# Kernel optimization log

Measured on AMD Instinct MI355X. Metric: run time of the kernel, lower is better.

Reference implementation:

```python
import jax, jax.numpy as jnp
import numpy as np

D_TENSOR = 64
SCALE = float(np.sqrt(D_TENSOR))


def setup_inputs() -> dict:
    key = jax.random.key(0)
    kq, kk, kv = jax.random.split(key, 3)
    shape = (1, 16, 4096, 64)  # [B, H, S, D]
    return {
        "q": jax.random.normal(kq, shape, dtype=jnp.float32),
        "k": jax.random.normal(kk, shape, dtype=jnp.float32),
        "v": jax.random.normal(kv, shape, dtype=jnp.float32),
    }


def reference(q, k, v):
    # attn = softmax(q @ k^T / sqrt(d)); output = attn @ v  (no mask, dropout=0/eval)
    scores = jnp.einsum("bhqd,bhkd->bhqk", q, k) / SCALE  # [B,H,S,S]
    attn = jax.nn.softmax(scores, axis=-1)
    output = jnp.einsum("bhqk,bhkd->bhqd", attn, v)       # [B,H,S,D]
    return (output, attn)
```

## Files before the change

### kernel.cpp

```cpp
#include <hip/hip_runtime.h>
#include <hip/hip_bf16.h>


#define NH  16
#define SEQ 4096
#define DH  64
#define BM  128
#define BN  64
#define NKT (SEQ / BN)
#define NRB (SEQ / BM)
#define NT  512

typedef __attribute__((ext_vector_type(8))) short bf16x8;
typedef __attribute__((ext_vector_type(4))) float f32x4;

static __device__ __forceinline__ unsigned short f2bf(float f) {
  unsigned x = __float_as_uint(f);
  return (unsigned short)((x + 0x7fffu + ((x >> 16) & 1u)) >> 16);
}

static __device__ __forceinline__ void bar_lgkm() {
  asm volatile("s_waitcnt lgkmcnt(0)" ::: "memory");
  __builtin_amdgcn_s_barrier();
  asm volatile("" ::: "memory");
}

static __device__ __forceinline__ int swz(int row, int col) {
  return row * 64 + (col ^ ((row & 7) << 3));
}


__global__ __launch_bounds__(NT, 4)
void attn_fused(const float* __restrict__ q, const float* __restrict__ kg,
                const float* __restrict__ vg, float* __restrict__ out,
                float* __restrict__ attn)
{
  __shared__ __align__(16) unsigned short Ks[2][64 * 64];
  __shared__ __align__(16) unsigned short Vt[2][64 * 64];
  __shared__ __align__(16) unsigned short Pb[4][32 * 64];

  const int nwg = NH * NRB;
  int bid = blockIdx.x;
  int wg = (bid & 7) * (nwg >> 3) + (bid >> 3);
  const int h    = wg >> 5;
  const int row0 = (wg & (NRB - 1)) * BM;

  const int t    = threadIdx.x;
  const int lane = t & 63;
  const int wid  = t >> 6;
  const int r16  = lane & 15;
  const int g4   = lane >> 4;
  const bool producer = (wid >= 4);

  const float* qh = q  + (size_t)h * SEQ * DH;
  const float* kh = kg + (size_t)h * SEQ * DH;
  const float* vh = vg + (size_t)h * SEQ * DH;

  const int pt = t - 256;
  const int pk = (pt & 255) >> 4;
  const int pd = (t & 15) * 4;

  bf16x8 qa[2][2];
  if (!producer) {
    const float QS = 0.125f * 1.44269504088896340736f;
    #pragma unroll
    for (int qf = 0; qf < 2; ++qf) {
      #pragma unroll
      for (int kf = 0; kf < 2; ++kf) {
        const float* qp = qh + (size_t)(row0 + wid * 32 + qf * 16 + r16) * DH + kf * 32 + g4 * 8;
        float4 x0 = *(const float4*)qp;
        float4 x1 = *(const float4*)(qp + 4);
        bf16x8 a;
        a[0] = (short)f2bf(x0.x * QS); a[1] = (short)f2bf(x0.y * QS);
        a[2] = (short)f2bf(x0.z * QS); a[3] = (short)f2bf(x0.w * QS);
        a[4] = (short)f2bf(x1.x * QS); a[5] = (short)f2bf(x1.y * QS);
        a[6] = (short)f2bf(x1.z * QS); a[7] = (short)f2bf(x1.w * QS);
        qa[qf][kf] = a;
      }
    }
  }

  float4 kr[4], vr[4];

  float rsum0 = 0.f, rsum1 = 0.f;

  if (producer) {
    #pragma unroll
    for (int i = 0; i < 4; ++i)
      kr[i] = *(const float4*)(kh + (size_t)(i * 16 + pk) * DH + pd);
    #pragma unroll
    for (int i = 0; i < 4; ++i)
      *(short4*)&Ks[0][swz(i * 16 + pk, pd)] =
          make_short4((short)f2bf(kr[i].x), (short)f2bf(kr[i].y),
                      (short)f2bf(kr[i].z), (short)f2bf(kr[i].w));
    #pragma unroll
    for (int i = 0; i < 4; ++i)
      kr[i] = *(const float4*)(kh + (size_t)(BN + i * 16 + pk) * DH + pd);
  }
  bar_lgkm();

  #pragma unroll 1
  for (int kt = 0; kt < NKT; ++kt) {
    if (producer) {
      if (kt < NKT - 1) {
        #pragma unroll
        for (int i = 0; i < 4; ++i)
          *(short4*)&Ks[(kt + 1) & 1][swz(i * 16 + pk, pd)] =
              make_short4((short)f2bf(kr[i].x), (short)f2bf(kr[i].y),
                          (short)f2bf(kr[i].z), (short)f2bf(kr[i].w));
        if (kt < NKT - 2) {
          #pragma unroll
          for (int i = 0; i < 4; ++i)
            kr[i] = *(const float4*)(kh + (size_t)((kt + 2) * BN + i * 16 + pk) * DH + pd);
        }
      }
    } else {
      const int b = kt & 1;
      #pragma unroll
      for (int n = 0; n < 4; ++n) {
        bf16x8 a0 = *(const bf16x8*)&Ks[b][swz(n * 16 + r16, g4 * 8)];
        bf16x8 a1 = *(const bf16x8*)&Ks[b][swz(n * 16 + r16, 32 + g4 * 8)];
        f32x4 c0 = {0.f, 0.f, 0.f, 0.f};
        f32x4 c1 = {0.f, 0.f, 0.f, 0.f};
        c0 = __builtin_amdgcn_mfma_f32_16x16x32_bf16(a0, qa[0][0], c0, 0, 0, 0);
        c0 = __builtin_amdgcn_mfma_f32_16x16x32_bf16(a1, qa[0][1], c0, 0, 0, 0);
        c1 = __builtin_amdgcn_mfma_f32_16x16x32_bf16(a0, qa[1][0], c1, 0, 0, 0);
        c1 = __builtin_amdgcn_mfma_f32_16x16x32_bf16(a1, qa[1][1], c1, 0, 0, 0);
        #pragma unroll
        for (int r = 0; r < 4; ++r) {
          rsum0 += __builtin_amdgcn_exp2f(c0[r]);
          rsum1 += __builtin_amdgcn_exp2f(c1[r]);
        }
      }
    }
    bar_lgkm();
  }

  float inv0 = 0.f, inv1 = 0.f;
  if (!producer) {
    rsum0 += __shfl_xor(rsum0, 16); rsum0 += __shfl_xor(rsum0, 32);
    rsum1 += __shfl_xor(rsum1, 16); rsum1 += __shfl_xor(rsum1, 32);
    inv0 = 1.0f / rsum0;
    inv1 = 1.0f / rsum1;
  }

  f32x4 accO[2][4];
  #pragma unroll
  for (int qf = 0; qf < 2; ++qf)
    #pragma unroll
    for (int n = 0; n < 4; ++n) accO[qf][n] = (f32x4){0.f, 0.f, 0.f, 0.f};

  if (producer) {
    #pragma unroll
    for (int i = 0; i < 4; ++i) {
      kr[i] = *(const float4*)(kh + (size_t)(i * 16 + pk) * DH + pd);
      vr[i] = *(const float4*)(vh + (size_t)(i * 16 + pk) * DH + pd);
    }
    #pragma unroll
    for (int i = 0; i < 4; ++i) {
      *(short4*)&Ks[0][swz(i * 16 + pk, pd)] =
          make_short4((short)f2bf(kr[i].x), (short)f2bf(kr[i].y),
                      (short)f2bf(kr[i].z), (short)f2bf(kr[i].w));
      Vt[0][swz(pd + 0, i * 16 + pk)] = f2bf(vr[i].x);
      Vt[0][swz(pd + 1, i * 16 + pk)] = f2bf(vr[i].y);
      Vt[0][swz(pd + 2, i * 16 + pk)] = f2bf(vr[i].z);
      Vt[0][swz(pd + 3, i * 16 + pk)] = f2bf(vr[i].w);
    }
    #pragma unroll
    for (int i = 0; i < 4; ++i) {
      kr[i] = *(const float4*)(kh + (size_t)(BN + i * 16 + pk) * DH + pd);
      vr[i] = *(const float4*)(vh + (size_t)(BN + i * 16 + pk) * DH + pd);
    }
  }
  bar_lgkm();

  float* ap0 = attn + (size_t)(h * SEQ + row0 + wid * 32 + r16) * SEQ;
  float* ap1 = ap0 + (size_t)16 * SEQ;

  #pragma unroll 1
  for (int kt = 0; kt < NKT; ++kt) {
    if (producer) {
      if (kt < NKT - 1) {
        const int b1 = (kt + 1) & 1;
        #pragma unroll
        for (int i = 0; i < 4; ++i) {
          *(short4*)&Ks[b1][swz(i * 16 + pk, pd)] =
              make_short4((short)f2bf(kr[i].x), (short)f2bf(kr[i].y),
                          (short)f2bf(kr[i].z), (short)f2bf(kr[i].w));
          Vt[b1][swz(pd + 0, i * 16 + pk)] = f2bf(vr[i].x);
          Vt[b1][swz(pd + 1, i * 16 + pk)] = f2bf(vr[i].y);
          Vt[b1][swz(pd + 2, i * 16 + pk)] = f2bf(vr[i].z);
          Vt[b1][swz(pd + 3, i * 16 + pk)] = f2bf(vr[i].w);
        }
        if (kt < NKT - 2) {
          #pragma unroll
          for (int i = 0; i < 4; ++i) {
            kr[i] = *(const float4*)(kh + (size_t)((kt + 2) * BN + i * 16 + pk) * DH + pd);
            vr[i] = *(const float4*)(vh + (size_t)((kt + 2) * BN + i * 16 + pk) * DH + pd);
          }
        }
      }
    } else {
      const int b = kt & 1;
      #pragma unroll
      for (int n = 0; n < 4; ++n) {
        bf16x8 a0 = *(const bf16x8*)&Ks[b][swz(n * 16 + r16, g4 * 8)];
        bf16x8 a1 = *(const bf16x8*)&Ks[b][swz(n * 16 + r16, 32 + g4 * 8)];
        f32x4 c0 = {0.f, 0.f, 0.f, 0.f};
        f32x4 c1 = {0.f, 0.f, 0.f, 0.f};
        c0 = __builtin_amdgcn_mfma_f32_16x16x32_bf16(a0, qa[0][0], c0, 0, 0, 0);
        c0 = __builtin_amdgcn_mfma_f32_16x16x32_bf16(a1, qa[0][1], c0, 0, 0, 0);
        c1 = __builtin_amdgcn_mfma_f32_16x16x32_bf16(a0, qa[1][0], c1, 0, 0, 0);
        c1 = __builtin_amdgcn_mfma_f32_16x16x32_bf16(a1, qa[1][1], c1, 0, 0, 0);
        f32x4 p0, p1;
        p0[0] = __builtin_amdgcn_exp2f(c0[0]) * inv0;
        p0[1] = __builtin_amdgcn_exp2f(c0[1]) * inv0;
        p0[2] = __builtin_amdgcn_exp2f(c0[2]) * inv0;
        p0[3] = __builtin_amdgcn_exp2f(c0[3]) * inv0;
        p1[0] = __builtin_amdgcn_exp2f(c1[0]) * inv1;
        p1[1] = __builtin_amdgcn_exp2f(c1[1]) * inv1;
        p1[2] = __builtin_amdgcn_exp2f(c1[2]) * inv1;
        p1[3] = __builtin_amdgcn_exp2f(c1[3]) * inv1;
        __builtin_nontemporal_store(p0, (f32x4*)(ap0 + (size_t)kt * BN + n * 16 + g4 * 4));
        __builtin_nontemporal_store(p1, (f32x4*)(ap1 + (size_t)kt * BN + n * 16 + g4 * 4));
        *(short4*)&Pb[wid][swz(r16, n * 16 + g4 * 4)] =
            make_short4((short)f2bf(p0[0]), (short)f2bf(p0[1]),
                        (short)f2bf(p0[2]), (short)f2bf(p0[3]));
        *(short4*)&Pb[wid][swz(16 + r16, n * 16 + g4 * 4)] =
            make_short4((short)f2bf(p1[0]), (short)f2bf(p1[1]),
                        (short)f2bf(p1[2]), (short)f2bf(p1[3]));
      }
      bf16x8 pa00 = *(const bf16x8*)&Pb[wid][swz(r16, g4 * 8)];
      bf16x8 pa01 = *(const bf16x8*)&Pb[wid][swz(r16, 32 + g4 * 8)];
      bf16x8 pa10 = *(const bf16x8*)&Pb[wid][swz(16 + r16, g4 * 8)];
      bf16x8 pa11 = *(const bf16x8*)&Pb[wid][swz(16 + r16, 32 + g4 * 8)];
      #pragma unroll
      for (int n = 0; n < 4; ++n) {
        bf16x8 v0 = *(const bf16x8*)&Vt[b][swz(n * 16 + r16, g4 * 8)];
        bf16x8 v1 = *(const bf16x8*)&Vt[b][swz(n * 16 + r16, 32 + g4 * 8)];
        accO[0][n] = __builtin_amdgcn_mfma_f32_16x16x32_bf16(pa00, v0, accO[0][n], 0, 0, 0);
        accO[0][n] = __builtin_amdgcn_mfma_f32_16x16x32_bf16(pa01, v1, accO[0][n], 0, 0, 0);
        accO[1][n] = __builtin_amdgcn_mfma_f32_16x16x32_bf16(pa10, v0, accO[1][n], 0, 0, 0);
        accO[1][n] = __builtin_amdgcn_mfma_f32_16x16x32_bf16(pa11, v1, accO[1][n], 0, 0, 0);
      }
    }
    bar_lgkm();
  }

  if (!producer) {
    #pragma unroll
    for (int qf = 0; qf < 2; ++qf) {
      #pragma unroll
      for (int n = 0; n < 4; ++n) {
        #pragma unroll
        for (int r = 0; r < 4; ++r) {
          __builtin_nontemporal_store(accO[qf][n][r],
              out + (size_t)(h * SEQ + row0 + wid * 32 + qf * 16 + g4 * 4 + r) * DH + n * 16 + r16);
        }
      }
    }
  }
}

extern "C" void kernel_launch(void* const* d_in, const int* in_sizes, int n_in,
                              void* d_out, int out_size, void* d_ws, size_t ws_size,
                              hipStream_t stream) {
  const float* q = (const float*)d_in[0];
  const float* k = (const float*)d_in[1];
  const float* v = (const float*)d_in[2];
  float* out  = (float*)d_out;
  float* attn = out + (size_t)NH * SEQ * DH;
  hipLaunchKernelGGL(attn_fused, dim3(NH * NRB), dim3(NT), 0, stream,
                     q, k, v, out, attn);
}
```

Before: 377.0 us.

## Drop producer/consumer warp split; all warps compute 256-row blocks and cooperatively load K/V

```diff
diff --git a/kernel.cpp b/kernel.cpp
--- a/kernel.cpp
+++ b/kernel.cpp
@@ -5,7 +5,7 @@
 #define NH  16
 #define SEQ 4096
 #define DH  64
-#define BM  128
+#define BM  256
 #define BN  64
 #define NKT (SEQ / BN)
 #define NRB (SEQ / BM)
@@ -37,12 +37,12 @@
 {
   __shared__ __align__(16) unsigned short Ks[2][64 * 64];
   __shared__ __align__(16) unsigned short Vt[2][64 * 64];
-  __shared__ __align__(16) unsigned short Pb[4][32 * 64];
+  __shared__ __align__(16) unsigned short Pb[8][32 * 64];
 
   const int nwg = NH * NRB;
   int bid = blockIdx.x;
   int wg = (bid & 7) * (nwg >> 3) + (bid >> 3);
-  const int h    = wg >> 5;
+  const int h    = wg >> 4;
   const int row0 = (wg & (NRB - 1)) * BM;
 
   const int t    = threadIdx.x;
@@ -50,72 +50,60 @@
   const int wid  = t >> 6;
   const int r16  = lane & 15;
   const int g4   = lane >> 4;
-  const bool producer = (wid >= 4);
+  const bool khalf = (wid < 4);
 
   const float* qh = q  + (size_t)h * SEQ * DH;
   const float* kh = kg + (size_t)h * SEQ * DH;
   const float* vh = vg + (size_t)h * SEQ * DH;
 
-  const int pt = t - 256;
-  const int pk = (pt & 255) >> 4;
-  const int pd = (t & 15) * 4;
-
+  const int kKey1 = t >> 4;
+  const int kD1   = (t & 15) * 4;
+
+  const int ku  = t & 255;
+  const int kk2 = ku >> 4;
+  const int kd2 = (ku & 15) * 4;
+  const int vk0 = (ku >> 4) * 4;
+  const int vd  = ku & 15;
+
+  const float QS = 0.125f * 1.44269504088896340736f;
   bf16x8 qa[2][2];
-  if (!producer) {
-    const float QS = 0.125f * 1.44269504088896340736f;
-    #pragma unroll
-    for (int qf = 0; qf < 2; ++qf) {
-      #pragma unroll
-      for (int kf = 0; kf < 2; ++kf) {
-        const float* qp = qh + (size_t)(row0 + wid * 32 + qf * 16 + r16) * DH + kf * 32 + g4 * 8;
-        float4 x0 = *(const float4*)qp;
-        float4 x1 = *(const float4*)(qp + 4);
-        bf16x8 a;
-        a[0] = (short)f2bf(x0.x * QS); a[1] = (short)f2bf(x0.y * QS);
-        a[2] = (short)f2bf(x0.z * QS); a[3] = (short)f2bf(x0.w * QS);
-        a[4] = (short)f2bf(x1.x * QS); a[5] = (short)f2bf(x1.y * QS);
-        a[6] = (short)f2bf(x1.z * QS); a[7] = (short)f2bf(x1.w * QS);
-        qa[qf][kf] = a;
-      }
-    }
-  }
-
-  float4 kr[4], vr[4];
+  #pragma unroll
+  for (int qf = 0; qf < 2; ++qf) {
+    #pragma unroll
+    for (int kf = 0; kf < 2; ++kf) {
+      const float* qp = qh + (size_t)(row0 + wid * 32 + qf * 16 + r16) * DH + kf * 32 + g4 * 8;
+      float4 x0 = *(const float4*)qp;
+      float4 x1 = *(const float4*)(qp + 4);
+      bf16x8 a;
+      a[0] = (short)f2bf(x0.x * QS); a[1] = (short)f2bf(x0.y * QS);
+      a[2] = (short)f2bf(x0.z * QS); a[3] = (short)f2bf(x0.w * QS);
+      a[4] = (short)f2bf(x1.x * QS); a[5] = (short)f2bf(x1.y * QS);
+      a[6] = (short)f2bf(x1.z * QS); a[7] = (short)f2bf(x1.w * QS);
+      qa[qf][kf] = a;
+    }
+  }
 
   float rsum0 = 0.f, rsum1 = 0.f;
-
-  if (producer) {
-    #pragma unroll
-    for (int i = 0; i < 4; ++i)
-      kr[i] = *(const float4*)(kh + (size_t)(i * 16 + pk) * DH + pd);
-    #pragma unroll
-    for (int i = 0; i < 4; ++i)
-      *(short4*)&Ks[0][swz(i * 16 + pk, pd)] =
-          make_short4((short)f2bf(kr[i].x), (short)f2bf(kr[i].y),
-                      (short)f2bf(kr[i].z), (short)f2bf(kr[i].w));
-    #pragma unroll
-    for (int i = 0; i < 4; ++i)
-      kr[i] = *(const float4*)(kh + (size_t)(BN + i * 16 + pk) * DH + pd);
-  }
-  bar_lgkm();
-
-  #pragma unroll 1
-  for (int kt = 0; kt < NKT; ++kt) {
-    if (producer) {
-      if (kt < NKT - 1) {
-        #pragma unroll
-        for (int i = 0; i < 4; ++i)
-          *(short4*)&Ks[(kt + 1) & 1][swz(i * 16 + pk, pd)] =
-              make_short4((short)f2bf(kr[i].x), (short)f2bf(kr[i].y),
-                          (short)f2bf(kr[i].z), (short)f2bf(kr[i].w));
-        if (kt < NKT - 2) {
-          #pragma unroll
-          for (int i = 0; i < 4; ++i)
-            kr[i] = *(const float4*)(kh + (size_t)((kt + 2) * BN + i * 16 + pk) * DH + pd);
-        }
-      }
-    } else {
+  {
+    float4 kr[2];
+    #pragma unroll
+    for (int i = 0; i < 2; ++i)
+      kr[i] = *(const float4*)(kh + (size_t)(kKey1 + 32 * i) * DH + kD1);
+
+    #pragma unroll 1
+    for (int kt = 0; kt < NKT; ++kt) {
       const int b = kt & 1;
+      #pragma unroll
+      for (int i = 0; i < 2; ++i)
+        *(short4*)&Ks[b][swz(kKey1 + 32 * i, kD1)] =
+            make_short4((short)f2bf(kr[i].x), (short)f2bf(kr[i].y),
+                        (short)f2bf(kr[i].z), (short)f2bf(kr[i].w));
+      if (kt + 1 < NKT) {
+        #pragma unroll
+        for (int i = 0; i < 2; ++i)
+          kr[i] = *(const float4*)(kh + (size_t)((kt + 1) * BN + kKey1 + 32 * i) * DH + kD1);
+      }
+      bar_lgkm();
       #pragma unroll
       for (int n = 0; n < 4; ++n) {
         bf16x8 a0 = *(const bf16x8*)&Ks[b][swz(n * 16 + r16, g4 * 8)];
@@ -132,17 +120,14 @@
           rsum1 += __builtin_amdgcn_exp2f(c1[r]);
         }
       }
-    }
-    bar_lgkm();
-  }
-
-  float inv0 = 0.f, inv1 = 0.f;
-  if (!producer) {
-    rsum0 += __shfl_xor(rsum0, 16); rsum0 += __shfl_xor(rsum0, 32);
-    rsum1 += __shfl_xor(rsum1, 16); rsum1 += __shfl_xor(rsum1, 32);
-    inv0 = 1.0f / rsum0;
-    inv1 = 1.0f / rsum1;
-  }
+      bar_lgkm();
+    }
+  }
+
+  rsum0 += __shfl_xor(rsum0, 16); rsum0 += __shfl_xor(rsum0, 32);
+  rsum1 += __shfl_xor(rsum1, 16); rsum1 += __shfl_xor(rsum1, 32);
+  const float inv0 = 1.0f / rsum0;
+  const float inv1 = 1.0f / rsum1;
 
   f32x4 accO[2][4];
   #pragma unroll
@@ -150,113 +135,108 @@
     #pragma unroll
     for (int n = 0; n < 4; ++n) accO[qf][n] = (f32x4){0.f, 0.f, 0.f, 0.f};
 
-  if (producer) {
-    #pragma unroll
-    for (int i = 0; i < 4; ++i) {
-      kr[i] = *(const float4*)(kh + (size_t)(i * 16 + pk) * DH + pd);
-      vr[i] = *(const float4*)(vh + (size_t)(i * 16 + pk) * DH + pd);
-    }
-    #pragma unroll
-    for (int i = 0; i < 4; ++i) {
-      *(short4*)&Ks[0][swz(i * 16 + pk, pd)] =
-          make_short4((short)f2bf(kr[i].x), (short)f2bf(kr[i].y),
-                      (short)f2bf(kr[i].z), (short)f2bf(kr[i].w));
-      Vt[0][swz(pd + 0, i * 16 + pk)] = f2bf(vr[i].x);
-      Vt[0][swz(pd + 1, i * 16 + pk)] = f2bf(vr[i].y);
-      Vt[0][swz(pd + 2, i * 16 + pk)] = f2bf(vr[i].z);
-      Vt[0][swz(pd + 3, i * 16 + pk)] = f2bf(vr[i].w);
-    }
-    #pragma unroll
-    for (int i = 0; i < 4; ++i) {
-      kr[i] = *(const float4*)(kh + (size_t)(BN + i * 16 + pk) * DH + pd);
-      vr[i] = *(const float4*)(vh + (size_t)(BN + i * 16 + pk) * DH + pd);
-    }
-  }
-  bar_lgkm();
+  float4 pre[4];
+  if (khalf) {
+    #pragma unroll
+    for (int i = 0; i < 4; ++i)
+      pre[i] = *(const float4*)(kh + (size_t)(kk2 + 16 * i) * DH + kd2);
+  } else {
+    #pragma unroll
+    for (int c = 0; c < 4; ++c) {
+      const float* vp = vh + (size_t)vk0 * DH + (vd + 16 * c);
+      pre[c].x = vp[0 * DH]; pre[c].y = vp[1 * DH];
+      pre[c].z = vp[2 * DH]; pre[c].w = vp[3 * DH];
+    }
+  }
+  __syncthreads();
 
   float* ap0 = attn + (size_t)(h * SEQ + row0 + wid * 32 + r16) * SEQ;
   float* ap1 = ap0 + (size_t)16 * SEQ;
 
   #pragma unroll 1
   for (int kt = 0; kt < NKT; ++kt) {
-    if (producer) {
-      if (kt < NKT - 1) {
-        const int b1 = (kt + 1) & 1;
-        #pragma unroll
-        for (int i = 0; i < 4; ++i) {
-          *(short4*)&Ks[b1][swz(i * 16 + pk, pd)] =
-              make_short4((short)f2bf(kr[i].x), (short)f2bf(kr[i].y),
-                          (short)f2bf(kr[i].z), (short)f2bf(kr[i].w));
-          Vt[b1][swz(pd + 0, i * 16 + pk)] = f2bf(vr[i].x);
-          Vt[b1][swz(pd + 1, i * 16 + pk)] = f2bf(vr[i].y);
-          Vt[b1][swz(pd + 2, i * 16 + pk)] = f2bf(vr[i].z);
-          Vt[b1][swz(pd + 3, i * 16 + pk)] = f2bf(vr[i].w);
+    const int b = kt & 1;
+    if (khalf) {
+      #pragma unroll
+      for (int i = 0; i < 4; ++i)
+        *(short4*)&Ks[b][swz(kk2 + 16 * i, kd2)] =
+            make_short4((short)f2bf(pre[i].x), (short)f2bf(pre[i].y),
+                        (short)f2bf(pre[i].z), (short)f2bf(pre[i].w));
+    } else {
+      #pragma unroll
+      for (int c = 0; c < 4; ++c)
+        *(short4*)&Vt[b][swz(vd + 16 * c, vk0)] =
+            make_short4((short)f2bf(pre[c].x), (short)f2bf(pre[c].y),
+                        (short)f2bf(pre[c].z), (short)f2bf(pre[c].w));
+    }
+    if (kt + 1 < NKT) {
+      if (khalf) {
+        #pragma unroll
+        for (int i = 0; i < 4; ++i)
+          pre[i] = *(const float4*)(kh + (size_t)((kt + 1) * BN + kk2 + 16 * i) * DH + kd2);
+      } else {
+        #pragma unroll
+        for (int c = 0; c < 4; ++c) {
+          const float* vp = vh + (size_t)((kt + 1) * BN + vk0) * DH + (vd + 16 * c);
+          pre[c].x = vp[0 * DH]; pre[c].y = vp[1 * DH];
+          pre[c].z = vp[2 * DH]; pre[c].w = vp[3 * DH];
         }
-        if (kt < NKT - 2) {
-          #pragma unroll
-          for (int i = 0; i < 4; ++i) {
-            kr[i] = *(const float4*)(kh + (size_t)((kt + 2) * BN + i * 16 + pk) * DH + pd);
-            vr[i] = *(const float4*)(vh + (size_t)((kt + 2) * BN + i * 16 + pk) * DH + pd);
-          }
-        }
-      }
-    } else {
-      const int b = kt & 1;
-      #pragma unroll
-      for (int n = 0; n < 4; ++n) {
-        bf16x8 a0 = *(const bf16x8*)&Ks[b][swz(n * 16 + r16, g4 * 8)];
-        bf16x8 a1 = *(const bf16x8*)&Ks[b][swz(n * 16 + r16, 32 + g4 * 8)];
-        f32x4 c0 = {0.f, 0.f, 0.f, 0.f};
-        f32x4 c1 = {0.f, 0.f, 0.f, 0.f};
-        c0 = __builtin_amdgcn_mfma_f32_16x16x32_bf16(a0, qa[0][0], c0, 0, 0, 0);
-        c0 = __builtin_amdgcn_mfma_f32_16x16x32_bf16(a1, qa[0][1], c0, 0, 0, 0);
-        c1 = __builtin_amdgcn_mfma_f32_16x16x32_bf16(a0, qa[1][0], c1, 0, 0, 0);
-        c1 = __builtin_amdgcn_mfma_f32_16x16x32_bf16(a1, qa[1][1], c1, 0, 0, 0);
-        f32x4 p0, p1;
-        p0[0] = __builtin_amdgcn_exp2f(c0[0]) * inv0;
-        p0[1] = __builtin_amdgcn_exp2f(c0[1]) * inv0;
-        p0[2] = __builtin_amdgcn_exp2f(c0[2]) * inv0;
-        p0[3] = __builtin_amdgcn_exp2f(c0[3]) * inv0;
-        p1[0] = __builtin_amdgcn_exp2f(c1[0]) * inv1;
-        p1[1] = __builtin_amdgcn_exp2f(c1[1]) * inv1;
-        p1[2] = __builtin_amdgcn_exp2f(c1[2]) * inv1;
-        p1[3] = __builtin_amdgcn_exp2f(c1[3]) * inv1;
-        __builtin_nontemporal_store(p0, (f32x4*)(ap0 + (size_t)kt * BN + n * 16 + g4 * 4));
-        __builtin_nontemporal_store(p1, (f32x4*)(ap1 + (size_t)kt * BN + n * 16 + g4 * 4));
-        *(short4*)&Pb[wid][swz(r16, n * 16 + g4 * 4)] =
-            make_short4((short)f2bf(p0[0]), (short)f2bf(p0[1]),
-                        (short)f2bf(p0[2]), (short)f2bf(p0[3]));
-        *(short4*)&Pb[wid][swz(16 + r16, n * 16 + g4 * 4)] =
-            make_short4((short)f2bf(p1[0]), (short)f2bf(p1[1]),
-                        (short)f2bf(p1[2]), (short)f2bf(p1[3]));
-      }
-      bf16x8 pa00 = *(const bf16x8*)&Pb[wid][swz(r16, g4 * 8)];
-      bf16x8 pa01 = *(const bf16x8*)&Pb[wid][swz(r16, 32 + g4 * 8)];
-      bf16x8 pa10 = *(const bf16x8*)&Pb[wid][swz(16 + r16, g4 * 8)];
-      bf16x8 pa11 = *(const bf16x8*)&Pb[wid][swz(16 + r16, 32 + g4 * 8)];
-      #pragma unroll
-      for (int n = 0; n < 4; ++n) {
-        bf16x8 v0 = *(const bf16x8*)&Vt[b][swz(n * 16 + r16, g4 * 8)];
-        bf16x8 v1 = *(const bf16x8*)&Vt[b][swz(n * 16 + r16, 32 + g4 * 8)];
-        accO[0][n] = __builtin_amdgcn_mfma_f32_16x16x32_bf16(pa00, v0, accO[0][n], 0, 0, 0);
-        accO[0][n] = __builtin_amdgcn_mfma_f32_16x16x32_bf16(pa01, v1, accO[0][n], 0, 0, 0);
-        accO[1][n] = __builtin_amdgcn_mfma_f32_16x16x32_bf16(pa10, v0, accO[1][n], 0, 0, 0);
-        accO[1][n] = __builtin_amdgcn_mfma_f32_16x16x32_bf16(pa11, v1, accO[1][n], 0, 0, 0);
       }
     }
     bar_lgkm();
-  }
-
-  if (!producer) {
-    #pragma unroll
-    for (int qf = 0; qf < 2; ++qf) {
-      #pragma unroll
-      for (int n = 0; n < 4; ++n) {
-        #pragma unroll
-        for (int r = 0; r < 4; ++r) {
-          __builtin_nontemporal_store(accO[qf][n][r],
-              out + (size_t)(h * SEQ + row0 + wid * 32 + qf * 16 + g4 * 4 + r) * DH + n * 16 + r16);
-        }
+
+    #pragma unroll
+    for (int n = 0; n < 4; ++n) {
+      bf16x8 a0 = *(const bf16x8*)&Ks[b][swz(n * 16 + r16, g4 * 8)];
+      bf16x8 a1 = *(const bf16x8*)&Ks[b][swz(n * 16 + r16, 32 + g4 * 8)];
+      f32x4 c0 = {0.f, 0.f, 0.f, 0.f};
+      f32x4 c1 = {0.f, 0.f, 0.f, 0.f};
+      c0 = __builtin_amdgcn_mfma_f32_16x16x32_bf16(a0, qa[0][0], c0, 0, 0, 0);
+      c0 = __builtin_amdgcn_mfma_f32_16x16x32_bf16(a1, qa[0][1], c0, 0, 0, 0);
+      c1 = __builtin_amdgcn_mfma_f32_16x16x32_bf16(a0, qa[1][0], c1, 0, 0, 0);
+      c1 = __builtin_amdgcn_mfma_f32_16x16x32_bf16(a1, qa[1][1], c1, 0, 0, 0);
+      f32x4 p0, p1;
+      p0[0] = __builtin_amdgcn_exp2f(c0[0]) * inv0;
+      p0[1] = __builtin_amdgcn_exp2f(c0[1]) * inv0;
+      p0[2] = __builtin_amdgcn_exp2f(c0[2]) * inv0;
+      p0[3] = __builtin_amdgcn_exp2f(c0[3]) * inv0;
+      p1[0] = __builtin_amdgcn_exp2f(c1[0]) * inv1;
+      p1[1] = __builtin_amdgcn_exp2f(c1[1]) * inv1;
+      p1[2] = __builtin_amdgcn_exp2f(c1[2]) * inv1;
+      p1[3] = __builtin_amdgcn_exp2f(c1[3]) * inv1;
+      __builtin_nontemporal_store(p0, (f32x4*)(ap0 + (size_t)kt * BN + n * 16 + g4 * 4));
+      __builtin_nontemporal_store(p1, (f32x4*)(ap1 + (size_t)kt * BN + n * 16 + g4 * 4));
+      *(short4*)&Pb[wid][swz(r16, n * 16 + g4 * 4)] =
+          make_short4((short)f2bf(p0[0]), (short)f2bf(p0[1]),
+                      (short)f2bf(p0[2]), (short)f2bf(p0[3]));
+      *(short4*)&Pb[wid][swz(16 + r16, n * 16 + g4 * 4)] =
+          make_short4((short)f2bf(p1[0]), (short)f2bf(p1[1]),
+                      (short)f2bf(p1[2]), (short)f2bf(p1[3]));
+    }
+    bf16x8 pa00 = *(const bf16x8*)&Pb[wid][swz(r16, g4 * 8)];
+    bf16x8 pa01 = *(const bf16x8*)&Pb[wid][swz(r16, 32 + g4 * 8)];
+    bf16x8 pa10 = *(const bf16x8*)&Pb[wid][swz(16 + r16, g4 * 8)];
+    bf16x8 pa11 = *(const bf16x8*)&Pb[wid][swz(16 + r16, 32 + g4 * 8)];
+    #pragma unroll
+    for (int n = 0; n < 4; ++n) {
+      bf16x8 v0 = *(const bf16x8*)&Vt[b][swz(n * 16 + r16, g4 * 8)];
+      bf16x8 v1 = *(const bf16x8*)&Vt[b][swz(n * 16 + r16, 32 + g4 * 8)];
+      accO[0][n] = __builtin_amdgcn_mfma_f32_16x16x32_bf16(pa00, v0, accO[0][n], 0, 0, 0);
+      accO[0][n] = __builtin_amdgcn_mfma_f32_16x16x32_bf16(pa01, v1, accO[0][n], 0, 0, 0);
+      accO[1][n] = __builtin_amdgcn_mfma_f32_16x16x32_bf16(pa10, v0, accO[1][n], 0, 0, 0);
+      accO[1][n] = __builtin_amdgcn_mfma_f32_16x16x32_bf16(pa11, v1, accO[1][n], 0, 0, 0);
+    }
+    bar_lgkm();
+  }
+
+  #pragma unroll
+  for (int qf = 0; qf < 2; ++qf) {
+    #pragma unroll
+    for (int n = 0; n < 4; ++n) {
+      #pragma unroll
+      for (int r = 0; r < 4; ++r) {
+        __builtin_nontemporal_store(accO[qf][n][r],
+            out + (size_t)(h * SEQ + row0 + wid * 32 + qf * 16 + g4 * 4 + r) * DH + n * 16 + r16);
       }
     }
   }
```

Result: slower. 403.6 us (+7.1%).
